# Kernel tuning notes

Measured on AMD Instinct MI355X. Metric: run time of the kernel, lower is better.

The kernel has to match this reference:

```python
import jax, jax.numpy as jnp
import numpy as np

B, T, D, E, K = 4, 2048, 2048, 8, 2
H = 4 * D  # expert hidden dim


def setup_inputs() -> dict:
    key = jax.random.key(0)
    ks = jax.random.split(key, 12)
    s = 0.02  # weight init scale
    return {
        "x": jax.random.normal(ks[0], (B, T, D), dtype=jnp.float32),
        "eps": jax.random.normal(ks[1], (B, T, E), dtype=jnp.float32),
        "Wr": jax.random.normal(ks[2], (D, E), dtype=jnp.float32) * s,
        "br": jnp.zeros((E,), dtype=jnp.float32),
        "Wn": jax.random.normal(ks[3], (D, E), dtype=jnp.float32) * s,
        "bn": jnp.zeros((E,), dtype=jnp.float32),
        "W1": jax.random.normal(ks[4], (E, D, H), dtype=jnp.float32) * s,
        "b1": jnp.zeros((E, H), dtype=jnp.float32),
        "W2": jax.random.normal(ks[5], (E, H, D), dtype=jnp.float32) * s,
        "b2": jnp.zeros((E, D), dtype=jnp.float32),
    }


def _moe(x, eps, Wr, br, Wn, bn, W1, b1, W2, b2):
    # --- noisy top-k router ---
    logits = x @ Wr + br                                   # [B,T,E]
    noise_logits = x @ Wn + bn                             # [B,T,E]
    noisy = logits + eps * jax.nn.softplus(noise_logits)   # [B,T,E]
    _, top_idx = jax.lax.top_k(noisy, K)                   # [B,T,K]
    sel = jax.nn.one_hot(top_idx, E, dtype=noisy.dtype).sum(-2)  # [B,T,E] 0/1
    neg_inf = jnp.asarray(-jnp.inf, dtype=noisy.dtype)
    sparse_logits = jnp.where(sel > 0, noisy, neg_inf)
    gates = jax.nn.softmax(sparse_logits, axis=-1)         # zeros off the top-k
    # --- expert MLPs, combined with gates (gate==0 exactly when unrouted,
    #     matching the torch masked gather/scatter; dropout in eval mode) ---
    out = jnp.zeros_like(x)
    for i in range(E):  # fixed small expert count
        h = jax.nn.relu(x @ W1[i] + b1[i])                 # [B,T,H]
        y = h @ W2[i] + b2[i]                              # [B,T,D]
        out = out + y * gates[..., i:i + 1]
    return out


def reference(x, eps, Wr, br, Wn, bn, W1, b1, W2, b2):
    return _moe(x, eps, Wr, br, Wn, bn, W1, b1, W2, b2)
```

## Files before the change

kernel.cpp:

```cpp
#include <hip/hip_runtime.h>

#define BT_TOK 8192
#define DDIM   2048
#define EEXP   8
#define HDIM   8192
#define MAXTILES 72

typedef __bf16 bf16x8 __attribute__((ext_vector_type(8)));
typedef float  f32x4  __attribute__((ext_vector_type(4)));

__device__ inline ushort f2bf(float f) {
  unsigned u = __float_as_uint(f);
  u += 0x7FFFu + ((u >> 16) & 1u);
  return (ushort)(u >> 16);
}

__device__ __forceinline__ void gl16(const ushort* g, ushort* l) {
  __builtin_amdgcn_global_load_lds(
      (const __attribute__((address_space(1))) void*)g,
      (__attribute__((address_space(3))) void*)l, 16, 0, 0);
}

__global__ __launch_bounds__(256) void k_router(
    const float* __restrict__ x, const float* __restrict__ eps,
    const float* __restrict__ Wr, const float* __restrict__ br,
    const float* __restrict__ Wn, const float* __restrict__ bn,
    int* __restrict__ cnt, int* __restrict__ tk_e, int* __restrict__ tk_p,
    float* __restrict__ tk_g)
{
  const int lane = threadIdx.x & 63;
  const int t = blockIdx.x * 4 + (threadIdx.x >> 6);
  const float* xr = x + (size_t)t * DDIM;
  float aL[8] = {0,0,0,0,0,0,0,0};
  float aN[8] = {0,0,0,0,0,0,0,0};
  for (int i = lane; i < DDIM; i += 64) {
    float xv = xr[i];
    const float4* wr4 = (const float4*)(Wr + (size_t)i * EEXP);
    const float4* wn4 = (const float4*)(Wn + (size_t)i * EEXP);
    float4 r0 = wr4[0], r1 = wr4[1];
    float4 n0 = wn4[0], n1 = wn4[1];
    aL[0] += xv * r0.x; aL[1] += xv * r0.y; aL[2] += xv * r0.z; aL[3] += xv * r0.w;
    aL[4] += xv * r1.x; aL[5] += xv * r1.y; aL[6] += xv * r1.z; aL[7] += xv * r1.w;
    aN[0] += xv * n0.x; aN[1] += xv * n0.y; aN[2] += xv * n0.z; aN[3] += xv * n0.w;
    aN[4] += xv * n1.x; aN[5] += xv * n1.y; aN[6] += xv * n1.z; aN[7] += xv * n1.w;
  }
  #pragma unroll
  for (int e = 0; e < 8; ++e) {
    float v = aL[e];
    #pragma unroll
    for (int s = 32; s; s >>= 1) v += __shfl_xor(v, s);
    aL[e] = v;
    float w = aN[e];
    #pragma unroll
    for (int s = 32; s; s >>= 1) w += __shfl_xor(w, s);
    aN[e] = w;
  }
  float nz[8];
  #pragma unroll
  for (int e = 0; e < 8; ++e) {
    float l = aL[e] + br[e];
    float z = aN[e] + bn[e];
    float sp = fmaxf(z, 0.f) + log1pf(expf(-fabsf(z)));
    nz[e] = l + eps[(size_t)t * EEXP + e] * sp;
  }
  int e1 = 0; float v1 = nz[0];
  #pragma unroll
  for (int e = 1; e < 8; ++e) if (nz[e] > v1) { v1 = nz[e]; e1 = e; }
  int e2 = (e1 == 0) ? 1 : 0; float v2 = nz[e2];
  #pragma unroll
  for (int e = 0; e < 8; ++e) if (e != e1 && nz[e] > v2) { v2 = nz[e]; e2 = e; }
  float ex = expf(v2 - v1);
  float g1 = 1.f / (1.f + ex);
  float g2 = ex / (1.f + ex);
  if (lane == 0) {
    int p1 = atomicAdd(&cnt[e1], 1);
    int p2 = atomicAdd(&cnt[e2], 1);
    tk_e[t * 2 + 0] = e1; tk_p[t * 2 + 0] = p1; tk_g[t * 2 + 0] = g1;
    tk_e[t * 2 + 1] = e2; tk_p[t * 2 + 1] = p2; tk_g[t * 2 + 1] = g2;
  }
}

__global__ void k_off(const int* __restrict__ cnt, int* __restrict__ off,
                      int* __restrict__ tileMap, int* __restrict__ nTiles) {
  if (threadIdx.x == 0 && blockIdx.x == 0) {
    int a = 0, nt = 0;
    for (int e = 0; e < EEXP; ++e) {
      off[e] = a;
      int mt = (cnt[e] + 255) >> 8;
      for (int m = 0; m < mt; ++m) tileMap[nt++] = (e << 16) | m;
      a += cnt[e];
    }
    off[EEXP] = a;
    nTiles[0] = nt;
  }
}

__global__ __launch_bounds__(256) void k_gather(
    const float* __restrict__ x, const int* __restrict__ off,
    const int* __restrict__ tk_e, const int* __restrict__ tk_p,
    const float* __restrict__ tk_g,
    int* __restrict__ tok, float* __restrict__ gate, ushort* __restrict__ xg)
{
  const int b = blockIdx.x;
  const int t = b >> 1;
  const int e = tk_e[b];
  const int slot = off[e] + tk_p[b];
  if (threadIdx.x == 0) { tok[slot] = t; gate[slot] = tk_g[b]; }
  const float4* src = (const float4*)(x + (size_t)t * DDIM);
  ushort* dst = xg + (size_t)slot * DDIM;
  const int i = threadIdx.x;
  float4 a = src[i * 2 + 0];
  float4 c = src[i * 2 + 1];
  union { ushort u[8]; uint4 q; } pk;
  pk.u[0] = f2bf(a.x); pk.u[1] = f2bf(a.y); pk.u[2] = f2bf(a.z); pk.u[3] = f2bf(a.w);
  pk.u[4] = f2bf(c.x); pk.u[5] = f2bf(c.y); pk.u[6] = f2bf(c.z); pk.u[7] = f2bf(c.w);
  *(uint4*)(dst + (size_t)i * 8) = pk.q;
}

__global__ __launch_bounds__(256) void k_transpose(
    const float* __restrict__ W, ushort* __restrict__ Wt, int R, int C)
{
  const int e = blockIdx.z;
  const float* We = W + (size_t)e * R * C;
  ushort* Wte = Wt + (size_t)e * R * C;
  const int r0 = blockIdx.y * 64, c0 = blockIdx.x * 64;
  __shared__ float tile[64][65];
  const int tx = threadIdx.x & 15, ty = threadIdx.x >> 4;
  #pragma unroll
  for (int p = 0; p < 4; ++p) {
    float4 v = *(const float4*)(We + (size_t)(r0 + p * 16 + ty) * C + c0 + tx * 4);
    tile[p * 16 + ty][tx * 4 + 0] = v.x;
    tile[p * 16 + ty][tx * 4 + 1] = v.y;
    tile[p * 16 + ty][tx * 4 + 2] = v.z;
    tile[p * 16 + ty][tx * 4 + 3] = v.w;
  }
  __syncthreads();
  const int c = threadIdx.x >> 2, rb = (threadIdx.x & 3) * 16;
  union { ushort u[16]; uint4 q[2]; } pk;
  #pragma unroll
  for (int j = 0; j < 16; ++j) pk.u[j] = f2bf(tile[rb + j][c]);
  uint4* dst = (uint4*)(Wte + (size_t)(c0 + c) * R + r0 + rb);
  dst[0] = pk.q[0];
  dst[1] = pk.q[1];
}


#define MFMA_(a, b, c) __builtin_amdgcn_mfma_f32_16x16x32_bf16(a, b, c, 0, 0, 0)
#define DSR(D, A) asm volatile("ds_read_b128 %0, %1" : "=v"(D) : "v"(A))

template<int KD, int EPI, int NDIM>
__global__ __launch_bounds__(512, 2) void k_gemm(
    const ushort* __restrict__ A, const ushort* __restrict__ B,
    const float* __restrict__ bias, const int* __restrict__ off,
    const int* __restrict__ tileMap, const int* __restrict__ nTiles,
    const int* __restrict__ tok, const float* __restrict__ gate,
    ushort* __restrict__ Hout, float* __restrict__ Out)
{
  constexpr int NKT = KD / 64;
  constexpr int NTN = NDIM / 256;
  __shared__ ushort lds[65536];
  const int TM = nTiles[0];
  const int T = TM * NTN;

  const int bid = blockIdx.x;
  const int xcd = bid & 7, slot = bid >> 3;
  const int qq = T >> 3, rr = T & 7;
  const int base = xcd * qq + (xcd < rr ? xcd : rr);
  const int csz = qq + (xcd < rr ? 1 : 0);

  const int tid = threadIdx.x;
  const int lane = tid & 63, wid = tid >> 6;
  const int wm = wid >> 2, wn = wid & 3;
  const int fr = lane & 15, q2 = lane >> 4;
  const unsigned lbase =
      (unsigned)(size_t)(__attribute__((address_space(3))) ushort*)lds;
  const int swz = (q2 ^ (fr & 7)) * 16;
  const int aoff0 = (int)lbase + wm * 16384 + fr * 128 + swz;
  const int boff0 = (int)lbase + 32768 + wn * 8192 + fr * 128 + swz;
  const int trow = tid >> 3;
  const int kx = ((tid & 7) ^ (trow & 7)) * 8;
  const int dstA = tid * 8;

#define STG(SRC, DUS) gl16((SRC), &lds[DUS])

  for (int it = slot; it < csz; it += 32) {
    const int f = base + it;
    const int ni = (int)((unsigned)f / (unsigned)TM);
    const int em = tileMap[f - ni * TM];
    const int e = em >> 16, mi = em & 0xffff;
    const int o = off[e], n_e = off[e + 1] - o;
    const int m0 = mi * 256;

    const ushort* Bex = B + (size_t)e * NDIM * KD + (size_t)ni * 256 * KD;
    const ushort* aS[4]; const ushort* bS[4];
    #pragma unroll
    for (int j = 0; j < 4; ++j) {
      int ar = m0 + j * 64 + trow;
      if (ar > n_e - 1) ar = n_e - 1;
      aS[j] = A + (size_t)(o + ar) * KD + kx;
      bS[j] = Bex + (size_t)(j * 64 + trow) * KD + kx;
    }

    f32x4 acc[8][4];
    #pragma unroll
    for (int m = 0; m < 8; ++m)
      #pragma unroll
      for (int n = 0; n < 4; ++n) acc[m][n] = (f32x4){0.f, 0.f, 0.f, 0.f};

    STG(aS[0], 0 + dstA);        STG(aS[2], 8192 + dstA);
    STG(aS[1], 4096 + dstA);     STG(aS[3], 12288 + dstA);
    STG(bS[0], 16384 + dstA);    STG(bS[1], 20480 + dstA);
    STG(bS[2], 24576 + dstA);    STG(bS[3], 28672 + dstA);
    if (NKT > 1) {
      STG(aS[0] + 64, 32768 + 0 + dstA);     STG(aS[2] + 64, 32768 + 8192 + dstA);
      STG(aS[1] + 64, 32768 + 4096 + dstA);  STG(aS[3] + 64, 32768 + 12288 + dstA);
      STG(bS[0] + 64, 32768 + 16384 + dstA); STG(bS[1] + 64, 32768 + 20480 + dstA);
      STG(bS[2] + 64, 32768 + 24576 + dstA); STG(bS[3] + 64, 32768 + 28672 + dstA);
      asm volatile("s_waitcnt vmcnt(8)");
    } else {
      asm volatile("s_waitcnt vmcnt(0)");
    }
    __builtin_amdgcn_s_barrier();
    __builtin_amdgcn_sched_barrier(0);

    #pragma unroll 1
    for (int t = 0; t < NKT; ++t) {
      const int bb = (t & 1) << 16;
      const int aA = aoff0 + bb;
      const int bA = boff0 + bb;
      const int cbu = (t & 1) * 32768;
      const size_t ko = (size_t)(t + 2) * 64;
      const bool pf = (t + 2 < NKT);

      bf16x8 avL[8], avH[8], bvL[4], bvH[4];

      #pragma unroll
      for (int i = 0; i < 4; ++i) {
        DSR(avL[2 * i],     aA + i * 2048);
        DSR(avL[2 * i + 1], (aA + i * 2048) ^ 64);
      }
      DSR(bvL[0], bA);         DSR(bvL[1], bA ^ 64);
      DSR(bvL[2], bA + 2048);  DSR(bvL[3], (bA + 2048) ^ 64);
      __builtin_amdgcn_s_barrier();
      asm volatile("s_waitcnt lgkmcnt(0)");
      __builtin_amdgcn_sched_barrier(0);
      __builtin_amdgcn_s_setprio(1);
      #pragma unroll
      for (int i = 0; i < 4; ++i) {
        acc[i][0] = MFMA_(avL[2 * i], bvL[0], acc[i][0]);
        acc[i][0] = MFMA_(avL[2 * i + 1], bvL[1], acc[i][0]);
        acc[i][1] = MFMA_(avL[2 * i], bvL[2], acc[i][1]);
        acc[i][1] = MFMA_(avL[2 * i + 1], bvL[3], acc[i][1]);
      }
      __builtin_amdgcn_s_setprio(0);
      __builtin_amdgcn_s_barrier();

      #pragma unroll
      for (int i = 0; i < 4; ++i) {
        DSR(avH[2 * i],     aA + 8192 + i * 2048);
        DSR(avH[2 * i + 1], (aA + 8192 + i * 2048) ^ 64);
      }
      if (pf) {
        STG(aS[0] + ko, cbu + 0 + dstA);
        STG(aS[2] + ko, cbu + 8192 + dstA);
      }
      __builtin_amdgcn_s_barrier();
      asm volatile("s_waitcnt lgkmcnt(0)");
      __builtin_amdgcn_sched_barrier(0);
      __builtin_amdgcn_s_setprio(1);
      #pragma unroll
      for (int i = 0; i < 4; ++i) {
        acc[4 + i][0] = MFMA_(avH[2 * i], bvL[0], acc[4 + i][0]);
        acc[4 + i][0] = MFMA_(avH[2 * i + 1], bvL[1], acc[4 + i][0]);
        acc[4 + i][1] = MFMA_(avH[2 * i], bvL[2], acc[4 + i][1]);
        acc[4 + i][1] = MFMA_(avH[2 * i + 1], bvL[3], acc[4 + i][1]);
      }
      __builtin_amdgcn_s_setprio(0);
      __builtin_amdgcn_s_barrier();

      DSR(bvH[0], bA + 4096);  DSR(bvH[1], (bA + 4096) ^ 64);
      DSR(bvH[2], bA + 6144);  DSR(bvH[3], (bA + 6144) ^ 64);
      if (pf) {
        STG(aS[1] + ko, cbu + 4096 + dstA);
        STG(aS[3] + ko, cbu + 12288 + dstA);
      }
      __builtin_amdgcn_s_barrier();
      asm volatile("s_waitcnt lgkmcnt(0)");
      __builtin_amdgcn_sched_barrier(0);
      __builtin_amdgcn_s_setprio(1);
      #pragma unroll
      for (int i = 0; i < 4; ++i) {
        acc[i][2] = MFMA_(avL[2 * i], bvH[0], acc[i][2]);
        acc[i][2] = MFMA_(avL[2 * i + 1], bvH[1], acc[i][2]);
        acc[i][3] = MFMA_(avL[2 * i], bvH[2], acc[i][3]);
        acc[i][3] = MFMA_(avL[2 * i + 1], bvH[3], acc[i][3]);
      }
      __builtin_amdgcn_s_setprio(0);
      __builtin_amdgcn_s_barrier();

      if (pf) {
        STG(bS[0] + ko, cbu + 16384 + dstA);
        STG(bS[1] + ko, cbu + 20480 + dstA);
        STG(bS[2] + ko, cbu + 24576 + dstA);
        STG(bS[3] + ko, cbu + 28672 + dstA);
      }
      __builtin_amdgcn_s_setprio(1);
      #pragma unroll
      for (int i = 0; i < 4; ++i) {
        acc[4 + i][2] = MFMA_(avH[2 * i], bvH[0], acc[4 + i][2]);
        acc[4 + i][2] = MFMA_(avH[2 * i + 1], bvH[1], acc[4 + i][2]);
        acc[4 + i][3] = MFMA_(avH[2 * i], bvH[2], acc[4 + i][3]);
        acc[4 + i][3] = MFMA_(avH[2 * i + 1], bvH[3], acc[4 + i][3]);
      }
      __builtin_amdgcn_s_setprio(0);
      __builtin_amdgcn_sched_barrier(0);
      if (t < NKT - 2) asm volatile("s_waitcnt vmcnt(8)");
      else             asm volatile("s_waitcnt vmcnt(0)");
      __builtin_amdgcn_s_barrier();
      __builtin_amdgcn_sched_barrier(0);
    }

    const int colBase = ni * 256 + wn * 64 + fr;
    const int rBase = m0 + wm * 128 + q2 * 4;
    float bb4[4];
    #pragma unroll
    for (int n = 0; n < 4; ++n) bb4[n] = bias[(size_t)e * NDIM + colBase + n * 16];

    if constexpr (EPI == 0) {
      #pragma unroll
      for (int m = 0; m < 8; ++m) {
        #pragma unroll
        for (int jj = 0; jj < 4; ++jj) {
          int r = rBase + m * 16 + jj;
          if (r < n_e) {
            ushort* hp = Hout + (size_t)(o + r) * NDIM + colBase;
            #pragma unroll
            for (int n = 0; n < 4; ++n)
              hp[n * 16] = f2bf(fmaxf(acc[m][n][jj] + bb4[n], 0.f));
          }
        }
      }
    } else {
      #pragma unroll
      for (int m = 0; m < 8; ++m) {
        #pragma unroll
        for (int jj = 0; jj < 4; ++jj) {
          int r = rBase + m * 16 + jj;
          if (r < n_e) {
            int tt = tok[o + r];
            float g = gate[o + r];
            float* op = Out + (size_t)tt * NDIM + colBase;
            #pragma unroll
            for (int n = 0; n < 4; ++n)
              atomicAdd(op + n * 16, g * (acc[m][n][jj] + bb4[n]));
          }
        }
      }
    }
  }
#undef STG
}

extern "C" void kernel_launch(void* const* d_in, const int* in_sizes, int n_in,
                              void* d_out, int out_size, void* d_ws, size_t ws_size,
                              hipStream_t stream) {
  const float* x   = (const float*)d_in[0];
  const float* eps = (const float*)d_in[1];
  const float* Wr  = (const float*)d_in[2];
  const float* br  = (const float*)d_in[3];
  const float* Wn  = (const float*)d_in[4];
  const float* bn  = (const float*)d_in[5];
  const float* W1  = (const float*)d_in[6];
  const float* b1  = (const float*)d_in[7];
  const float* W2  = (const float*)d_in[8];
  const float* b2  = (const float*)d_in[9];
  float* out = (float*)d_out;

  char* p = (char*)d_ws;
  size_t used = 0;
  auto alloc = [&](size_t bytes) -> void* {
    void* r = p + used;
    used += (bytes + 255) & ~(size_t)255;
    return r;
  };
  int*    cnt   = (int*)alloc(EEXP * 4);
  int*    off   = (int*)alloc((EEXP + 1) * 4);
  int*    tmap  = (int*)alloc(MAXTILES * 4);
  int*    ntl   = (int*)alloc(4);
  int*    tk_e  = (int*)alloc(2 * BT_TOK * 4);
  int*    tk_p  = (int*)alloc(2 * BT_TOK * 4);
  float*  tk_g  = (float*)alloc(2 * BT_TOK * 4);
  int*    tok   = (int*)alloc(2 * BT_TOK * 4);
  float*  gate  = (float*)alloc(2 * BT_TOK * 4);
  ushort* xg    = (ushort*)alloc((size_t)2 * BT_TOK * DDIM * 2);
  ushort* Wt1   = (ushort*)alloc((size_t)EEXP * HDIM * DDIM * 2);
  ushort* Wt2   = (ushort*)alloc((size_t)EEXP * HDIM * DDIM * 2);
  ushort* hbuf  = (ushort*)alloc((size_t)2 * BT_TOK * HDIM * 2);
  if (used > ws_size) return;

  hipMemsetAsync(d_out, 0, (size_t)out_size * 4, stream);
  hipMemsetAsync(cnt, 0, EEXP * 4, stream);

  k_router<<<BT_TOK / 4, 256, 0, stream>>>(x, eps, Wr, br, Wn, bn,
                                           cnt, tk_e, tk_p, tk_g);
  k_off<<<1, 64, 0, stream>>>(cnt, off, tmap, ntl);
  k_gather<<<2 * BT_TOK, 256, 0, stream>>>(x, off, tk_e, tk_p, tk_g, tok, gate, xg);

  {
    dim3 g1(HDIM / 64, DDIM / 64, EEXP);
    k_transpose<<<g1, 256, 0, stream>>>(W1, Wt1, DDIM, HDIM);
    dim3 g2(DDIM / 64, HDIM / 64, EEXP);
    k_transpose<<<g2, 256, 0, stream>>>(W2, Wt2, HDIM, DDIM);
  }

  {
    k_gemm<DDIM, 0, HDIM><<<256, 512, 0, stream>>>(xg, Wt1, b1, off, tmap, ntl,
                                                   tok, gate, hbuf, out);
    k_gemm<HDIM, 1, DDIM><<<256, 512, 0, stream>>>(hbuf, Wt2, b2, off, tmap, ntl,
                                                   tok, gate, hbuf, out);
  }
}
```

Before: 1.918 ms.

## Split-K second expert GEMM, drop atomics via combine kernel, prefetch LDS fragments

The second GEMM is split into two K-halves to double the tile count for better occupancy, which matters because few M-tiles exist. Each half writes gated partial results per slot into a scratch buffer that reuses the Wt1 memory. A new combine kernel sums the four partials per token, replacing the float atomicAdd scatter and the output memset. The GEMM main loop is also re-pipelined so the next step's LDS fragments load during the last MFMA quarter and waits are relaxed to partial lgkmcnt. The cost is extra traffic for the fp32 partial buffer and one more kernel launch.

```diff
diff --git a/kernel.cpp b/kernel.cpp
--- a/kernel.cpp
+++ b/kernel.cpp
@@ -4,7 +4,8 @@
 #define DDIM   2048
 #define EEXP   8
 #define HDIM   8192
-#define MAXTILES 72
+#define MAXT1  72
+#define MAXT2  144
 
 typedef __bf16 bf16x8 __attribute__((ext_vector_type(8)));
 typedef float  f32x4  __attribute__((ext_vector_type(4)));
@@ -81,17 +82,22 @@
 }
 
 __global__ void k_off(const int* __restrict__ cnt, int* __restrict__ off,
-                      int* __restrict__ tileMap, int* __restrict__ nTiles) {
+                      int* __restrict__ tm1, int* __restrict__ tm2,
+                      int* __restrict__ ntl) {
   if (threadIdx.x == 0 && blockIdx.x == 0) {
-    int a = 0, nt = 0;
+    int a = 0, n1 = 0, n2 = 0;
     for (int e = 0; e < EEXP; ++e) {
       off[e] = a;
       int mt = (cnt[e] + 255) >> 8;
-      for (int m = 0; m < mt; ++m) tileMap[nt++] = (e << 16) | m;
+      for (int m = 0; m < mt; ++m) {
+        tm1[n1++] = (e << 8) | (m << 1);
+        tm2[n2++] = (e << 8) | (m << 1);
+        tm2[n2++] = (e << 8) | (m << 1) | 1;
+      }
       a += cnt[e];
     }
     off[EEXP] = a;
-    nTiles[0] = nt;
+    ntl[0] = n1; ntl[1] = n2;
   }
 }
 
@@ -99,13 +105,13 @@
     const float* __restrict__ x, const int* __restrict__ off,
     const int* __restrict__ tk_e, const int* __restrict__ tk_p,
     const float* __restrict__ tk_g,
-    int* __restrict__ tok, float* __restrict__ gate, ushort* __restrict__ xg)
+    int* __restrict__ slt, float* __restrict__ gate, ushort* __restrict__ xg)
 {
   const int b = blockIdx.x;
   const int t = b >> 1;
   const int e = tk_e[b];
   const int slot = off[e] + tk_p[b];
-  if (threadIdx.x == 0) { tok[slot] = t; gate[slot] = tk_g[b]; }
+  if (threadIdx.x == 0) { slt[b] = slot; gate[slot] = tk_g[b]; }
   const float4* src = (const float4*)(x + (size_t)t * DDIM);
   ushort* dst = xg + (size_t)slot * DDIM;
   const int i = threadIdx.x;
@@ -147,23 +153,33 @@
 
 #define MFMA_(a, b, c) __builtin_amdgcn_mfma_f32_16x16x32_bf16(a, b, c, 0, 0, 0)
 #define DSR(D, A) asm volatile("ds_read_b128 %0, %1" : "=v"(D) : "v"(A))
-
-template<int KD, int EPI, int NDIM>
+#define MQ(MB, NB, AV, BV) do {                                                  \
+    _Pragma("unroll")                                                            \
+    for (int i_ = 0; i_ < 4; ++i_) {                                             \
+      acc[(MB)+i_][(NB)]   = MFMA_(AV[2*i_],   BV[0], acc[(MB)+i_][(NB)]);       \
+      acc[(MB)+i_][(NB)]   = MFMA_(AV[2*i_+1], BV[1], acc[(MB)+i_][(NB)]);       \
+      acc[(MB)+i_][(NB)+1] = MFMA_(AV[2*i_],   BV[2], acc[(MB)+i_][(NB)+1]);     \
+      acc[(MB)+i_][(NB)+1] = MFMA_(AV[2*i_+1], BV[3], acc[(MB)+i_][(NB)+1]);     \
+    }                                                                            \
+  } while (0)
+
+template<int KD, int KSPLIT, int EPI, int NDIM>
 __global__ __launch_bounds__(512, 2) void k_gemm(
     const ushort* __restrict__ A, const ushort* __restrict__ B,
     const float* __restrict__ bias, const int* __restrict__ off,
-    const int* __restrict__ tileMap, const int* __restrict__ nTiles,
-    const int* __restrict__ tok, const float* __restrict__ gate,
-    ushort* __restrict__ Hout, float* __restrict__ Out)
+    const int* __restrict__ tileMap, const int* __restrict__ nT,
+    const float* __restrict__ gate,
+    ushort* __restrict__ Hout, float* __restrict__ Y)
 {
-  constexpr int NKT = KD / 64;
+  constexpr int KS = KD / KSPLIT;
+  constexpr int NKT = KS / 64;
   constexpr int NTN = NDIM / 256;
   __shared__ ushort lds[65536];
-  const int TM = nTiles[0];
+  const int TM = nT[0];
   const int T = TM * NTN;
 
   const int bid = blockIdx.x;
-  const int xcd = bid & 7, slot = bid >> 3;
+  const int xcd = bid & 7, sl = bid >> 3;
   const int qq = T >> 3, rr = T & 7;
   const int base = xcd * qq + (xcd < rr ? xcd : rr);
   const int csz = qq + (xcd < rr ? 1 : 0);
@@ -183,22 +199,23 @@
 
 #define STG(SRC, DUS) gl16((SRC), &lds[DUS])
 
-  for (int it = slot; it < csz; it += 32) {
+  for (int it = sl; it < csz; it += 32) {
     const int f = base + it;
     const int ni = (int)((unsigned)f / (unsigned)TM);
-    const int em = tileMap[f - ni * TM];
-    const int e = em >> 16, mi = em & 0xffff;
+    const int pk = tileMap[f - ni * TM];
+    const int e = pk >> 8, mi = (pk >> 1) & 127, kh = pk & 1;
     const int o = off[e], n_e = off[e + 1] - o;
     const int m0 = mi * 256;
-
-    const ushort* Bex = B + (size_t)e * NDIM * KD + (size_t)ni * 256 * KD;
+    const int k0 = kh * KS;
+
+    const ushort* Bex = B + (size_t)e * NDIM * KD + (size_t)ni * 256 * KD + k0 + kx;
     const ushort* aS[4]; const ushort* bS[4];
     #pragma unroll
     for (int j = 0; j < 4; ++j) {
       int ar = m0 + j * 64 + trow;
       if (ar > n_e - 1) ar = n_e - 1;
-      aS[j] = A + (size_t)(o + ar) * KD + kx;
-      bS[j] = Bex + (size_t)(j * 64 + trow) * KD + kx;
+      aS[j] = A + (size_t)(o + ar) * KD + k0 + kx;
+      bS[j] = Bex + (size_t)(j * 64 + trow) * KD;
     }
 
     f32x4 acc[8][4];
@@ -207,21 +224,28 @@
       #pragma unroll
       for (int n = 0; n < 4; ++n) acc[m][n] = (f32x4){0.f, 0.f, 0.f, 0.f};
 
+    bf16x8 avL[8], avH[8], bvL[4], bvH[4];
+
     STG(aS[0], 0 + dstA);        STG(aS[2], 8192 + dstA);
     STG(aS[1], 4096 + dstA);     STG(aS[3], 12288 + dstA);
     STG(bS[0], 16384 + dstA);    STG(bS[1], 20480 + dstA);
     STG(bS[2], 24576 + dstA);    STG(bS[3], 28672 + dstA);
-    if (NKT > 1) {
-      STG(aS[0] + 64, 32768 + 0 + dstA);     STG(aS[2] + 64, 32768 + 8192 + dstA);
-      STG(aS[1] + 64, 32768 + 4096 + dstA);  STG(aS[3] + 64, 32768 + 12288 + dstA);
-      STG(bS[0] + 64, 32768 + 16384 + dstA); STG(bS[1] + 64, 32768 + 20480 + dstA);
-      STG(bS[2] + 64, 32768 + 24576 + dstA); STG(bS[3] + 64, 32768 + 28672 + dstA);
-      asm volatile("s_waitcnt vmcnt(8)");
-    } else {
-      asm volatile("s_waitcnt vmcnt(0)");
-    }
+    STG(aS[0] + 64, 32768 + 0 + dstA);     STG(aS[2] + 64, 32768 + 8192 + dstA);
+    STG(aS[1] + 64, 32768 + 4096 + dstA);  STG(aS[3] + 64, 32768 + 12288 + dstA);
+    STG(bS[0] + 64, 32768 + 16384 + dstA); STG(bS[1] + 64, 32768 + 20480 + dstA);
+    STG(bS[2] + 64, 32768 + 24576 + dstA); STG(bS[3] + 64, 32768 + 28672 + dstA);
+    asm volatile("s_waitcnt vmcnt(8)");
     __builtin_amdgcn_s_barrier();
     __builtin_amdgcn_sched_barrier(0);
+    {
+      const int aA = aoff0, bA = boff0;
+      DSR(avL[0], aA);        DSR(avL[1], aA ^ 64);
+      DSR(avL[2], aA + 2048); DSR(avL[3], (aA + 2048) ^ 64);
+      DSR(avL[4], aA + 4096); DSR(avL[5], (aA + 4096) ^ 64);
+      DSR(avL[6], aA + 6144); DSR(avL[7], (aA + 6144) ^ 64);
+      DSR(bvL[0], bA);        DSR(bvL[1], bA ^ 64);
+      DSR(bvL[2], bA + 2048); DSR(bvL[3], (bA + 2048) ^ 64);
+    }
 
     #pragma unroll 1
     for (int t = 0; t < NKT; ++t) {
@@ -232,99 +256,72 @@
       const size_t ko = (size_t)(t + 2) * 64;
       const bool pf = (t + 2 < NKT);
 
-      bf16x8 avL[8], avH[8], bvL[4], bvH[4];
-
-      #pragma unroll
-      for (int i = 0; i < 4; ++i) {
-        DSR(avL[2 * i],     aA + i * 2048);
-        DSR(avL[2 * i + 1], (aA + i * 2048) ^ 64);
-      }
-      DSR(bvL[0], bA);         DSR(bvL[1], bA ^ 64);
-      DSR(bvL[2], bA + 2048);  DSR(bvL[3], (bA + 2048) ^ 64);
+      DSR(avH[0], aA + 8192);         DSR(avH[1], (aA + 8192) ^ 64);
+      DSR(avH[2], aA + 10240);        DSR(avH[3], (aA + 10240) ^ 64);
+      DSR(avH[4], aA + 12288);        DSR(avH[5], (aA + 12288) ^ 64);
+      DSR(avH[6], aA + 14336);        DSR(avH[7], (aA + 14336) ^ 64);
+      __builtin_amdgcn_s_barrier();
+      asm volatile("s_waitcnt lgkmcnt(8)");
+      __builtin_amdgcn_sched_barrier(0);
+      if (pf) { STG(aS[0] + ko, cbu + 0 + dstA); STG(aS[2] + ko, cbu + 8192 + dstA); }
+      __builtin_amdgcn_s_setprio(1);
+      MQ(0, 0, avL, bvL);
+      __builtin_amdgcn_s_setprio(0);
+      __builtin_amdgcn_s_barrier();
+
+      DSR(bvH[0], bA + 4096);  DSR(bvH[1], (bA + 4096) ^ 64);
+      DSR(bvH[2], bA + 6144);  DSR(bvH[3], (bA + 6144) ^ 64);
+      __builtin_amdgcn_s_barrier();
+      asm volatile("s_waitcnt lgkmcnt(4)");
+      __builtin_amdgcn_sched_barrier(0);
+      if (pf) { STG(aS[1] + ko, cbu + 4096 + dstA); STG(aS[3] + ko, cbu + 12288 + dstA); }
+      __builtin_amdgcn_s_setprio(1);
+      MQ(4, 0, avH, bvL);
+      __builtin_amdgcn_s_setprio(0);
+      __builtin_amdgcn_s_barrier();
+
       __builtin_amdgcn_s_barrier();
       asm volatile("s_waitcnt lgkmcnt(0)");
       __builtin_amdgcn_sched_barrier(0);
-      __builtin_amdgcn_s_setprio(1);
-      #pragma unroll
-      for (int i = 0; i < 4; ++i) {
-        acc[i][0] = MFMA_(avL[2 * i], bvL[0], acc[i][0]);
-        acc[i][0] = MFMA_(avL[2 * i + 1], bvL[1], acc[i][0]);
-        acc[i][1] = MFMA_(avL[2 * i], bvL[2], acc[i][1]);
-        acc[i][1] = MFMA_(avL[2 * i + 1], bvL[3], acc[i][1]);
-      }
-      __builtin_amdgcn_s_setprio(0);
-      __builtin_amdgcn_s_barrier();
-
-      #pragma unroll
-      for (int i = 0; i < 4; ++i) {
-        DSR(avH[2 * i],     aA + 8192 + i * 2048);
-        DSR(avH[2 * i + 1], (aA + 8192 + i * 2048) ^ 64);
-      }
       if (pf) {
-        STG(aS[0] + ko, cbu + 0 + dstA);
-        STG(aS[2] + ko, cbu + 8192 + dstA);
-      }
-      __builtin_amdgcn_s_barrier();
-      asm volatile("s_waitcnt lgkmcnt(0)");
-      __builtin_amdgcn_sched_barrier(0);
-      __builtin_amdgcn_s_setprio(1);
-      #pragma unroll
-      for (int i = 0; i < 4; ++i) {
-        acc[4 + i][0] = MFMA_(avH[2 * i], bvL[0], acc[4 + i][0]);
-        acc[4 + i][0] = MFMA_(avH[2 * i + 1], bvL[1], acc[4 + i][0]);
-        acc[4 + i][1] = MFMA_(avH[2 * i], bvL[2], acc[4 + i][1]);
-        acc[4 + i][1] = MFMA_(avH[2 * i + 1], bvL[3], acc[4 + i][1]);
-      }
-      __builtin_amdgcn_s_setprio(0);
-      __builtin_amdgcn_s_barrier();
-
-      DSR(bvH[0], bA + 4096);  DSR(bvH[1], (bA + 4096) ^ 64);
-      DSR(bvH[2], bA + 6144);  DSR(bvH[3], (bA + 6144) ^ 64);
-      if (pf) {
-        STG(aS[1] + ko, cbu + 4096 + dstA);
-        STG(aS[3] + ko, cbu + 12288 + dstA);
-      }
-      __builtin_amdgcn_s_barrier();
-      asm volatile("s_waitcnt lgkmcnt(0)");
-      __builtin_amdgcn_sched_barrier(0);
-      __builtin_amdgcn_s_setprio(1);
-      #pragma unroll
-      for (int i = 0; i < 4; ++i) {
-        acc[i][2] = MFMA_(avL[2 * i], bvH[0], acc[i][2]);
-        acc[i][2] = MFMA_(avL[2 * i + 1], bvH[1], acc[i][2]);
-        acc[i][3] = MFMA_(avL[2 * i], bvH[2], acc[i][3]);
-        acc[i][3] = MFMA_(avL[2 * i + 1], bvH[3], acc[i][3]);
-      }
-      __builtin_amdgcn_s_setprio(0);
-      __builtin_amdgcn_s_barrier();
-
-      if (pf) {
-        STG(bS[0] + ko, cbu + 16384 + dstA);
-        STG(bS[1] + ko, cbu + 20480 + dstA);
-        STG(bS[2] + ko, cbu + 24576 + dstA);
-        STG(bS[3] + ko, cbu + 28672 + dstA);
+        STG(bS[0] + ko, cbu + 16384 + dstA); STG(bS[1] + ko, cbu + 20480 + dstA);
+        STG(bS[2] + ko, cbu + 24576 + dstA); STG(bS[3] + ko, cbu + 28672 + dstA);
       }
       __builtin_amdgcn_s_setprio(1);
-      #pragma unroll
-      for (int i = 0; i < 4; ++i) {
-        acc[4 + i][2] = MFMA_(avH[2 * i], bvH[0], acc[4 + i][2]);
-        acc[4 + i][2] = MFMA_(avH[2 * i + 1], bvH[1], acc[4 + i][2]);
-        acc[4 + i][3] = MFMA_(avH[2 * i], bvH[2], acc[4 + i][3]);
-        acc[4 + i][3] = MFMA_(avH[2 * i + 1], bvH[3], acc[4 + i][3]);
+      MQ(0, 2, avL, bvH);
+      __builtin_amdgcn_s_setprio(0);
+      __builtin_amdgcn_s_barrier();
+
+      if (pf) asm volatile("s_waitcnt vmcnt(8)");
+      else    asm volatile("s_waitcnt vmcnt(0)");
+      __builtin_amdgcn_s_barrier();
+      __builtin_amdgcn_sched_barrier(0);
+      if (t + 1 < NKT) {
+        const int aN = aoff0 + (((t + 1) & 1) << 16);
+        const int bN = boff0 + (((t + 1) & 1) << 16);
+        DSR(avL[0], aN);        DSR(avL[1], aN ^ 64);
+        DSR(avL[2], aN + 2048); DSR(avL[3], (aN + 2048) ^ 64);
+        DSR(avL[4], aN + 4096); DSR(avL[5], (aN + 4096) ^ 64);
+        DSR(avL[6], aN + 6144); DSR(avL[7], (aN + 6144) ^ 64);
+        DSR(bvL[0], bN);        DSR(bvL[1], bN ^ 64);
+        DSR(bvL[2], bN + 2048); DSR(bvL[3], (bN + 2048) ^ 64);
       }
+      __builtin_amdgcn_s_setprio(1);
+      MQ(4, 2, avH, bvH);
       __builtin_amdgcn_s_setprio(0);
-      __builtin_amdgcn_sched_barrier(0);
-      if (t < NKT - 2) asm volatile("s_waitcnt vmcnt(8)");
-      else             asm volatile("s_waitcnt vmcnt(0)");
-      __builtin_amdgcn_s_barrier();
-      __builtin_amdgcn_sched_barrier(0);
+      __builtin_amdgcn_s_barrier();
     }
 
     const int colBase = ni * 256 + wn * 64 + fr;
     const int rBase = m0 + wm * 128 + q2 * 4;
     float bb4[4];
     #pragma unroll
-    for (int n = 0; n < 4; ++n) bb4[n] = bias[(size_t)e * NDIM + colBase + n * 16];
+    for (int n = 0; n < 4; ++n) {
+      if constexpr (EPI == 0)
+        bb4[n] = bias[(size_t)e * NDIM + colBase + n * 16];
+      else
+        bb4[n] = (kh == 0) ? bias[(size_t)e * NDIM + colBase + n * 16] : 0.f;
+    }
 
     if constexpr (EPI == 0) {
       #pragma unroll
@@ -341,24 +338,48 @@
         }
       }
     } else {
+      float* yk = Y + ((size_t)kh << 25);
       #pragma unroll
       for (int m = 0; m < 8; ++m) {
         #pragma unroll
         for (int jj = 0; jj < 4; ++jj) {
           int r = rBase + m * 16 + jj;
           if (r < n_e) {
-            int tt = tok[o + r];
             float g = gate[o + r];
-            float* op = Out + (size_t)tt * NDIM + colBase;
+            float* yp = yk + (size_t)(o + r) * NDIM + colBase;
             #pragma unroll
             for (int n = 0; n < 4; ++n)
-              atomicAdd(op + n * 16, g * (acc[m][n][jj] + bb4[n]));
+              yp[n * 16] = g * (acc[m][n][jj] + bb4[n]);
           }
         }
       }
     }
   }
 #undef STG
+}
+
+__global__ __launch_bounds__(256) void k_combine(
+    const float* __restrict__ Y, const int* __restrict__ slt,
+    float* __restrict__ out)
+{
+  const int t = blockIdx.x;
+  const int c = threadIdx.x * 8;
+  const int sA = slt[t * 2], sB = slt[t * 2 + 1];
+  const float4* pA0 = (const float4*)(Y + (size_t)sA * DDIM + c);
+  const float4* pB0 = (const float4*)(Y + (size_t)sB * DDIM + c);
+  const float4* pA1 = (const float4*)(Y + ((size_t)1 << 25) + (size_t)sA * DDIM + c);
+  const float4* pB1 = (const float4*)(Y + ((size_t)1 << 25) + (size_t)sB * DDIM + c);
+  float4* op = (float4*)(out + (size_t)t * DDIM + c);
+  #pragma unroll
+  for (int j = 0; j < 2; ++j) {
+    float4 a = pA0[j], b = pA1[j], cc = pB0[j], d = pB1[j];
+    float4 r;
+    r.x = a.x + b.x + cc.x + d.x;
+    r.y = a.y + b.y + cc.y + d.y;
+    r.z = a.z + b.z + cc.z + d.z;
+    r.w = a.w + b.w + cc.w + d.w;
+    op[j] = r;
+  }
 }
 
 extern "C" void kernel_launch(void* const* d_in, const int* in_sizes, int n_in,
@@ -385,26 +406,27 @@
   };
   int*    cnt   = (int*)alloc(EEXP * 4);
   int*    off   = (int*)alloc((EEXP + 1) * 4);
-  int*    tmap  = (int*)alloc(MAXTILES * 4);
-  int*    ntl   = (int*)alloc(4);
+  int*    tm1   = (int*)alloc(MAXT1 * 4);
+  int*    tm2   = (int*)alloc(MAXT2 * 4);
+  int*    ntl   = (int*)alloc(2 * 4);
   int*    tk_e  = (int*)alloc(2 * BT_TOK * 4);
   int*    tk_p  = (int*)alloc(2 * BT_TOK * 4);
   float*  tk_g  = (float*)alloc(2 * BT_TOK * 4);
-  int*    tok   = (int*)alloc(2 * BT_TOK * 4);
+  int*    slt   = (int*)alloc(2 * BT_TOK * 4);
   float*  gate  = (float*)alloc(2 * BT_TOK * 4);
   ushort* xg    = (ushort*)alloc((size_t)2 * BT_TOK * DDIM * 2);
   ushort* Wt1   = (ushort*)alloc((size_t)EEXP * HDIM * DDIM * 2);
   ushort* Wt2   = (ushort*)alloc((size_t)EEXP * HDIM * DDIM * 2);
   ushort* hbuf  = (ushort*)alloc((size_t)2 * BT_TOK * HDIM * 2);
   if (used > ws_size) return;
-
-  hipMemsetAsync(d_out, 0, (size_t)out_size * 4, stream);
+  float* Yf = (float*)Wt1;
+
   hipMemsetAsync(cnt, 0, EEXP * 4, stream);
 
   k_router<<<BT_TOK / 4, 256, 0, stream>>>(x, eps, Wr, br, Wn, bn,
                                            cnt, tk_e, tk_p, tk_g);
-  k_off<<<1, 64, 0, stream>>>(cnt, off, tmap, ntl);
-  k_gather<<<2 * BT_TOK, 256, 0, stream>>>(x, off, tk_e, tk_p, tk_g, tok, gate, xg);
+  k_off<<<1, 64, 0, stream>>>(cnt, off, tm1, tm2, ntl);
+  k_gather<<<2 * BT_TOK, 256, 0, stream>>>(x, off, tk_e, tk_p, tk_g, slt, gate, xg);
 
   {
     dim3 g1(HDIM / 64, DDIM / 64, EEXP);
@@ -413,10 +435,9 @@
     k_transpose<<<g2, 256, 0, stream>>>(W2, Wt2, HDIM, DDIM);
   }
 
-  {
-    k_gemm<DDIM, 0, HDIM><<<256, 512, 0, stream>>>(xg, Wt1, b1, off, tmap, ntl,
-                                                   tok, gate, hbuf, out);
-    k_gemm<HDIM, 1, DDIM><<<256, 512, 0, stream>>>(hbuf, Wt2, b2, off, tmap, ntl,
-                                                   tok, gate, hbuf, out);
-  }
-}
+  k_gemm<DDIM, 1, 0, HDIM><<<256, 512, 0, stream>>>(xg, Wt1, b1, off, tm1, ntl,
+                                                    gate, hbuf, Yf);
+  k_gemm<HDIM, 2, 1, DDIM><<<256, 512, 0, stream>>>(hbuf, Wt2, b2, off, tm2, ntl + 1,
+                                                    gate, hbuf, Yf);
+  k_combine<<<BT_TOK, 256, 0, stream>>>(Yf, slt, out);
+}
```

Measured after the change: 1.794 ms. 6.5% less time.
